# Kernel tuning notes

Hardware: AMD Instinct MI355X
Metric: run time of the kernel (lower is better)

The kernel has to match this reference:

```python
import jax, jax.numpy as jnp
import numpy as np

RATIO = 0.5  # SAGPooling ratio


def setup_inputs() -> dict:
    key = jax.random.key(0)
    ks = jax.random.split(key, 6)
    B, n, d, out_dim, Eg = 128, 512, 256, 256, 4096  # graphs, nodes/graph, feat, proj out, edges/graph
    N = B * n
    x = jax.random.normal(ks[0], (N, d), dtype=jnp.float32)
    # edges connect nodes within the same graph (contiguous node blocks)
    src = jax.random.randint(ks[1], (B, Eg), 0, n)
    dst = jax.random.randint(ks[2], (B, Eg), 0, n)
    off = (jnp.arange(B) * n)[:, None]
    edge_index = jnp.stack([(src + off).reshape(-1), (dst + off).reshape(-1)]).astype(jnp.int32)
    batch = jnp.repeat(jnp.arange(B), n).astype(jnp.int32)
    s = 1.0 / np.sqrt(d).astype(np.float32)
    w_rel = jax.random.normal(ks[3], (d, 1), dtype=jnp.float32) * s   # GraphConv lin_rel (has bias)
    b_rel = jnp.zeros((1,), dtype=jnp.float32)
    w_root = jax.random.normal(ks[4], (d, 1), dtype=jnp.float32) * s  # GraphConv lin_root (no bias)
    w_proj = jax.random.normal(ks[5], (d, out_dim), dtype=jnp.float32) * s  # projection Linear
    b_proj = jnp.zeros((out_dim,), dtype=jnp.float32)
    return {"x": x, "edge_index": edge_index, "batch": batch, "num_graphs": B,
            "w_rel": w_rel, "b_rel": b_rel, "w_root": w_root,
            "w_proj": w_proj, "b_proj": b_proj}


def reference(x, edge_index, batch, num_graphs, w_rel, b_rel, w_root, w_proj, b_proj):
    N, d = x.shape
    n = N // num_graphs                    # equal-size graphs
    k = int(np.ceil(RATIO * n))            # PyG topk: ceil(ratio * num_nodes)
    src, dst = edge_index[0], edge_index[1]
    # GraphConv(node_dim, 1): score_i = lin_rel(sum_{j->i} x_j) + lin_root(x_i)
    agg = jax.ops.segment_sum(x[src], dst, num_segments=N)          # [N, d]
    score = jnp.tanh((agg @ w_rel + b_rel + x @ w_root)[:, 0])       # [N], tanh nonlinearity
    sb = score.reshape(num_graphs, n)                                # [B, n]
    top_vals, top_idx = jax.lax.top_k(sb, k)                         # per-graph topk
    xb = x.reshape(num_graphs, n, d)
    x_sel = jnp.take_along_axis(xb, top_idx[:, :, None], axis=1)     # [B, k, d]
    x_sel = x_sel * top_vals[:, :, None]                             # x[perm] * score[perm] (multiplier=1)
    pooled = x_sel.mean(axis=1)                                      # global_mean_pool over k kept nodes
    return pooled @ w_proj + b_proj                                  # [B, out_dim]
```

## Files before the change

kernel.cpp:

```cpp
#include <hip/hip_runtime.h>

#define D        256
#define NPG      512
#define BG       128
#define KSEL     256
#define EPG      4096
#define NN       (BG * NPG)
#define ET       (BG * EPG)

__global__ __launch_bounds__(256) void k_proj_scores(
        const float* __restrict__ x,
        const float* __restrict__ w_rel, const float* __restrict__ w_root,
        float* __restrict__ p, float* __restrict__ r,
        float* __restrict__ pooled) {
    int tid  = threadIdx.x;
    int wave = tid >> 6, lane = tid & 63;
    int node = blockIdx.x * 4 + wave;

    if (blockIdx.x < BG) pooled[(size_t)blockIdx.x * D + tid] = 0.f;

    const float4* x4  = (const float4*)(x + (size_t)node * D);
    const float4* wr4 = (const float4*)w_rel;
    const float4* wo4 = (const float4*)w_root;
    float4 xv = x4[lane];
    float4 wr = wr4[lane];
    float4 wo = wo4[lane];
    float pv = xv.x * wr.x + xv.y * wr.y + xv.z * wr.z + xv.w * wr.w;
    float rv = xv.x * wo.x + xv.y * wo.y + xv.z * wo.z + xv.w * wo.w;
    #pragma unroll
    for (int off = 32; off; off >>= 1) {
        pv += __shfl_xor(pv, off, 64);
        rv += __shfl_xor(rv, off, 64);
    }
    if (lane == 0) { p[node] = pv; r[node] = rv; }
}

__global__ __launch_bounds__(512) void k_score_select(
        const int* __restrict__ ei,
        const float* __restrict__ p, const float* __restrict__ r,
        const float* __restrict__ b_rel,
        int* __restrict__ sel_idx, float* __restrict__ sel_val) {
    __shared__ float s_agg[NPG];
    __shared__ float s_val[NPG];
    __shared__ int   s_cnt;
    int b = blockIdx.x, tid = threadIdx.x;
    int base = b * NPG;

    s_agg[tid] = 0.f;
    if (tid == 0) s_cnt = 0;
    __syncthreads();

    const int* src = ei + (size_t)b * EPG;
    const int* dst = ei + ET + (size_t)b * EPG;
    #pragma unroll
    for (int e = tid; e < EPG; e += 512) {
        int si = src[e];
        int di = dst[e];
        atomicAdd(&s_agg[di - base], p[si]);
    }
    __syncthreads();

    float brel = b_rel[0];
    float sv = tanhf(s_agg[tid] + brel + r[base + tid]);
    s_val[tid] = sv;
    __syncthreads();

    int cnt = 0;
    for (int i = 0; i < NPG; ++i) {
        float o = s_val[i];
        cnt += (o > sv) || (o == sv && i < tid);
    }
    if (cnt < KSEL) {
        int pos = atomicAdd(&s_cnt, 1);
        sel_idx[b * KSEL + pos] = base + tid;
        sel_val[b * KSEL + pos] = sv;
    }
}

__global__ __launch_bounds__(256) void k_pool(
        const float* __restrict__ x,
        const int* __restrict__ sel_idx, const float* __restrict__ sel_val,
        float* __restrict__ pooled) {
    __shared__ int   s_i[64];
    __shared__ float s_v[64];
    int b = blockIdx.x, q = blockIdx.y, tid = threadIdx.x;
    if (tid < 64) {
        s_i[tid] = sel_idx[b * KSEL + q * 64 + tid];
        s_v[tid] = sel_val[b * KSEL + q * 64 + tid];
    }
    __syncthreads();
    float acc = 0.f;
    #pragma unroll 8
    for (int m = 0; m < 64; ++m) {
        acc += s_v[m] * x[(size_t)s_i[m] * D + tid];
    }
    atomicAdd(&pooled[b * D + tid], acc);
}

__global__ __launch_bounds__(256) void k_out(
        const float* __restrict__ pooled,
        const float* __restrict__ w_proj, const float* __restrict__ b_proj,
        float* __restrict__ out) {
    __shared__ float s_p[D];
    int b = blockIdx.x, tid = threadIdx.x;
    s_p[tid] = pooled[(size_t)b * D + tid] * (1.0f / KSEL);
    __syncthreads();
    float acc = b_proj[tid];
    #pragma unroll 8
    for (int kk = 0; kk < D; ++kk)
        acc += s_p[kk] * w_proj[kk * D + tid];
    out[(size_t)b * D + tid] = acc;
}

extern "C" void kernel_launch(void* const* d_in, const int* in_sizes, int n_in,
                              void* d_out, int out_size, void* d_ws, size_t ws_size,
                              hipStream_t stream) {
    const float* x      = (const float*)d_in[0];
    const int*   ei     = (const int*)d_in[1];
    const float* w_rel  = (const float*)d_in[4];
    const float* b_rel  = (const float*)d_in[5];
    const float* w_root = (const float*)d_in[6];
    const float* w_proj = (const float*)d_in[7];
    const float* b_proj = (const float*)d_in[8];
    float* out = (float*)d_out;

    float* p       = (float*)d_ws;
    float* r       = p + NN;
    float* pooled  = r + NN;
    float* sel_val = pooled + (size_t)BG * D;
    int*   sel_idx = (int*)(sel_val + (size_t)BG * KSEL);

    k_proj_scores<<<NN / 4, 256, 0, stream>>>(x, w_rel, w_root, p, r, pooled);
    k_score_select<<<BG, 512, 0, stream>>>(ei, p, r, b_rel, sel_idx, sel_val);
    k_pool<<<dim3(BG, 4), 256, 0, stream>>>(x, sel_idx, sel_val, pooled);
    k_out<<<BG, 256, 0, stream>>>(pooled, w_proj, b_proj, out);
}
```

Baseline: 145.3 us.

## Fuse score, top-k selection, pooling and projection into one per-graph kernel

Replaces the score/select, pool and output-projection kernels with a single 1024-thread block per graph that keeps scores, selected indices, pooled features and partial projections in shared memory. The rank count is split across two thread halves, and the pooled gather and projection are spread over 16 and 4 waves. This removes two launches, the global round-trips for selection and pooled results, and the global atomics. In exchange it runs only 128 blocks, so parallelism for the gather of x rows and the w_proj reads drops compared with the previous 512-block pool grid.

```diff
diff --git a/kernel.cpp b/kernel.cpp
--- a/kernel.cpp
+++ b/kernel.cpp
@@ -11,13 +11,10 @@
 __global__ __launch_bounds__(256) void k_proj_scores(
         const float* __restrict__ x,
         const float* __restrict__ w_rel, const float* __restrict__ w_root,
-        float* __restrict__ p, float* __restrict__ r,
-        float* __restrict__ pooled) {
+        float* __restrict__ p, float* __restrict__ r) {
     int tid  = threadIdx.x;
     int wave = tid >> 6, lane = tid & 63;
     int node = blockIdx.x * 4 + wave;
-
-    if (blockIdx.x < BG) pooled[(size_t)blockIdx.x * D + tid] = 0.f;
 
     const float4* x4  = (const float4*)(x + (size_t)node * D);
     const float4* wr4 = (const float4*)w_rel;
@@ -35,81 +32,101 @@
     if (lane == 0) { p[node] = pv; r[node] = rv; }
 }
 
-__global__ __launch_bounds__(512) void k_score_select(
-        const int* __restrict__ ei,
+__global__ __launch_bounds__(1024) void k_fused(
+        const float* __restrict__ x, const int* __restrict__ ei,
         const float* __restrict__ p, const float* __restrict__ r,
         const float* __restrict__ b_rel,
-        int* __restrict__ sel_idx, float* __restrict__ sel_val) {
+        const float* __restrict__ w_proj, const float* __restrict__ b_proj,
+        float* __restrict__ out) {
+    __shared__ float s_p[NPG];
+    __shared__ float s_r[NPG];
     __shared__ float s_agg[NPG];
     __shared__ float s_val[NPG];
-    __shared__ int   s_cnt;
+    __shared__ int   s_cnt2[1024];
+    __shared__ int   s_selid[KSEL];
+    __shared__ float s_selv[KSEL];
+    __shared__ float s_pool[D];
+    __shared__ float s_red[4][D];
+    __shared__ int   s_nsel;
+
     int b = blockIdx.x, tid = threadIdx.x;
     int base = b * NPG;
 
-    s_agg[tid] = 0.f;
-    if (tid == 0) s_cnt = 0;
+    if (tid < NPG) { s_p[tid] = p[base + tid]; s_agg[tid] = 0.f; }
+    else           { int j = tid - NPG; s_r[j] = r[base + j]; }
+    if (tid < D)   s_pool[tid] = 0.f;
+    if (tid == 0)  s_nsel = 0;
     __syncthreads();
 
     const int* src = ei + (size_t)b * EPG;
     const int* dst = ei + ET + (size_t)b * EPG;
     #pragma unroll
-    for (int e = tid; e < EPG; e += 512) {
-        int si = src[e];
-        int di = dst[e];
-        atomicAdd(&s_agg[di - base], p[si]);
+    for (int e = tid; e < EPG; e += 1024)
+        atomicAdd(&s_agg[dst[e] - base], s_p[src[e] - base]);
+    __syncthreads();
+
+    float brel = b_rel[0];
+    if (tid < NPG)
+        s_val[tid] = tanhf(s_agg[tid] + brel + s_r[tid]);
+    __syncthreads();
+
+    {
+        int j = tid & (NPG - 1);
+        int half = tid >> 9;
+        float sv = s_val[j];
+        int lo = half * 256;
+        int c = 0;
+        #pragma unroll 8
+        for (int i = lo; i < lo + 256; ++i) {
+            float o = s_val[i];
+            c += (o > sv) || (o == sv && i < j);
+        }
+        s_cnt2[tid] = c;
+    }
+    __syncthreads();
+    if (tid < NPG) {
+        int rank = s_cnt2[tid] + s_cnt2[tid + NPG];
+        if (rank < KSEL) {
+            int pos = atomicAdd(&s_nsel, 1);
+            s_selid[pos] = tid;
+            s_selv[pos]  = s_val[tid];
+        }
     }
     __syncthreads();
 
-    float brel = b_rel[0];
-    float sv = tanhf(s_agg[tid] + brel + r[base + tid]);
-    s_val[tid] = sv;
+    {
+        int wave = tid >> 6, lane = tid & 63;
+        float4 acc = {0.f, 0.f, 0.f, 0.f};
+        #pragma unroll 4
+        for (int m = 0; m < 16; ++m) {
+            int s   = wave * 16 + m;
+            int row = s_selid[s];
+            float v = s_selv[s];
+            float4 xv = ((const float4*)(x + (size_t)(base + row) * D))[lane];
+            acc.x += v * xv.x; acc.y += v * xv.y;
+            acc.z += v * xv.z; acc.w += v * xv.w;
+        }
+        atomicAdd(&s_pool[lane * 4 + 0], acc.x);
+        atomicAdd(&s_pool[lane * 4 + 1], acc.y);
+        atomicAdd(&s_pool[lane * 4 + 2], acc.z);
+        atomicAdd(&s_pool[lane * 4 + 3], acc.w);
+    }
     __syncthreads();
 
-    int cnt = 0;
-    for (int i = 0; i < NPG; ++i) {
-        float o = s_val[i];
-        cnt += (o > sv) || (o == sv && i < tid);
-    }
-    if (cnt < KSEL) {
-        int pos = atomicAdd(&s_cnt, 1);
-        sel_idx[b * KSEL + pos] = base + tid;
-        sel_val[b * KSEL + pos] = sv;
-    }
-}
-
-__global__ __launch_bounds__(256) void k_pool(
-        const float* __restrict__ x,
-        const int* __restrict__ sel_idx, const float* __restrict__ sel_val,
-        float* __restrict__ pooled) {
-    __shared__ int   s_i[64];
-    __shared__ float s_v[64];
-    int b = blockIdx.x, q = blockIdx.y, tid = threadIdx.x;
-    if (tid < 64) {
-        s_i[tid] = sel_idx[b * KSEL + q * 64 + tid];
-        s_v[tid] = sel_val[b * KSEL + q * 64 + tid];
+    {
+        int f = tid & (D - 1);
+        int q = tid >> 8;
+        float partial = 0.f;
+        int k0 = q * 64;
+        #pragma unroll 8
+        for (int kk = k0; kk < k0 + 64; ++kk)
+            partial += s_pool[kk] * w_proj[kk * D + f];
+        s_red[q][f] = partial;
     }
     __syncthreads();
-    float acc = 0.f;
-    #pragma unroll 8
-    for (int m = 0; m < 64; ++m) {
-        acc += s_v[m] * x[(size_t)s_i[m] * D + tid];
-    }
-    atomicAdd(&pooled[b * D + tid], acc);
-}
-
-__global__ __launch_bounds__(256) void k_out(
-        const float* __restrict__ pooled,
-        const float* __restrict__ w_proj, const float* __restrict__ b_proj,
-        float* __restrict__ out) {
-    __shared__ float s_p[D];
-    int b = blockIdx.x, tid = threadIdx.x;
-    s_p[tid] = pooled[(size_t)b * D + tid] * (1.0f / KSEL);
-    __syncthreads();
-    float acc = b_proj[tid];
-    #pragma unroll 8
-    for (int kk = 0; kk < D; ++kk)
-        acc += s_p[kk] * w_proj[kk * D + tid];
-    out[(size_t)b * D + tid] = acc;
+    if (tid < D)
+        out[(size_t)b * D + tid] = b_proj[tid] +
+            (s_red[0][tid] + s_red[1][tid] + s_red[2][tid] + s_red[3][tid]) * (1.0f / KSEL);
 }
 
 extern "C" void kernel_launch(void* const* d_in, const int* in_sizes, int n_in,
@@ -124,14 +141,9 @@
     const float* b_proj = (const float*)d_in[8];
     float* out = (float*)d_out;
 
-    float* p       = (float*)d_ws;
-    float* r       = p + NN;
-    float* pooled  = r + NN;
-    float* sel_val = pooled + (size_t)BG * D;
-    int*   sel_idx = (int*)(sel_val + (size_t)BG * KSEL);
+    float* p = (float*)d_ws;
+    float* r = p + NN;
 
-    k_proj_scores<<<NN / 4, 256, 0, stream>>>(x, w_rel, w_root, p, r, pooled);
-    k_score_select<<<BG, 512, 0, stream>>>(ei, p, r, b_rel, sel_idx, sel_val);
-    k_pool<<<dim3(BG, 4), 256, 0, stream>>>(x, sel_idx, sel_val, pooled);
-    k_out<<<BG, 256, 0, stream>>>(pooled, w_proj, b_proj, out);
+    k_proj_scores<<<NN / 4, 256, 0, stream>>>(x, w_rel, w_root, p, r);
+    k_fused<<<BG, 1024, 0, stream>>>(x, ei, p, r, b_rel, w_proj, b_proj, out);
 }
```

Measured after the change: 137.1 us. 5.7% less time.
